# Kernel optimization log

Measured on AMD Instinct MI355X. Metric: run time of the kernel, lower is better.

The kernel has to match this reference:

```python
import jax, jax.numpy as jnp
import numpy as np

SHORT_LEN = 10
NEG_INF = -1.0e9


def _attn_pool(values, user, w, w_bias, extra_b, mask, softmax_axis):
    # values: [B,L,D], user: [B,D]; linear+bias+relu, dot with user, masked softmax, weighted sum
    h = jax.nn.relu(jnp.einsum('bld,ed->ble', values, w) + w_bias + extra_b)
    s = jnp.einsum('bld,bd->bl', h, user)
    s = jnp.where(mask, NEG_INF, s)
    a = jax.nn.softmax(s, axis=softmax_axis)
    return jnp.einsum('bld,bl->bd', values, a)


def setup_inputs() -> dict:
    key = jax.random.key(0)
    ks = jax.random.split(key, 10)
    B, L, D, NI, NU = 2048, 50, 64, 100000, 100000
    return {
        'seq': jax.random.randint(ks[0], (B, L), 0, NI),
        'user_id': jax.random.randint(ks[1], (B,), 0, NU),
        'item_emb': jax.random.normal(ks[2], (NI, D), jnp.float32) * 0.01,
        'user_emb': jax.random.normal(ks[3], (NU, D), jnp.float32) * 0.01,
        'long_w': jax.random.normal(ks[4], (D, D), jnp.float32) * 0.1,
        'long_w_bias': jax.random.normal(ks[5], (D,), jnp.float32) * 0.1,
        'long_b': jax.random.normal(ks[6], (D,), jnp.float32) * 0.1,
        'long_short_w': jax.random.normal(ks[7], (D, D), jnp.float32) * 0.1,
        'long_short_w_bias': jax.random.normal(ks[8], (D,), jnp.float32) * 0.1,
        'long_short_b': jax.random.normal(ks[9], (D,), jnp.float32) * 0.1,
    }


def reference(seq, user_id, item_emb, user_emb, long_w, long_w_bias, long_b,
              long_short_w, long_short_w_bias, long_short_b):
    e = item_emb[seq]                     # [B,L,D]
    u = user_emb[user_id]                 # [B,D]
    mask = seq == 0                       # padding mask
    # long-term attention pooling (softmax over dim=1)
    long_term = _attn_pool(e, u, long_w, long_w_bias, long_b, mask, 1)[:, None, :]  # [B,1,D]
    # concat long-term summary with last SHORT_LEN items
    short = e[:, -SHORT_LEN:, :]
    mask_ls = jnp.concatenate([jnp.zeros((seq.shape[0], 1), bool), mask[:, -SHORT_LEN:]], axis=1)
    ls = jnp.concatenate([long_term, short], axis=1)  # [B,1+K,D]
    pooled = _attn_pool(ls, u, long_short_w, long_short_w_bias, long_short_b, mask_ls, -1)  # [B,D]
    scores = pooled @ item_emb.T          # [B, n_items]
    return scores
```

## Files before the change

### kernel.cpp

```cpp
#include <hip/hip_runtime.h>
#include <hip/hip_bf16.h>


#define L_SEQ 50
#define D_EMB 64
#define SHORT_LEN 10
#define LS_LEN 11
#define NEG_INF_F (-1000000000.0f)
#define TILE_STRIP 16

typedef __bf16 bf16x8 __attribute__((ext_vector_type(8)));
typedef float f32x4 __attribute__((ext_vector_type(4)));

__device__ __forceinline__ float wave_sum(float v) {
#pragma unroll
  for (int off = 32; off > 0; off >>= 1) v += __shfl_xor(v, off, 64);
  return v;
}
__device__ __forceinline__ float wave_max(float v) {
#pragma unroll
  for (int off = 32; off > 0; off >>= 1) v = fmaxf(v, __shfl_xor(v, off, 64));
  return v;
}

__global__ __launch_bounds__(64) void pool_kernel(
    const int* __restrict__ seq, const int* __restrict__ user_id,
    const float* __restrict__ item_emb, const float* __restrict__ user_emb,
    const float* __restrict__ w1, const float* __restrict__ w1b, const float* __restrict__ b1,
    const float* __restrict__ w2, const float* __restrict__ w2b, const float* __restrict__ b2,
    float* __restrict__ pooled_f32, __bf16* __restrict__ pooled_bf) {
  const int b = blockIdx.x;
  const int lane = threadIdx.x;

  __shared__ float e_lds[L_SEQ][D_EMB];
  __shared__ float ls_lds[LS_LEN][D_EMB];
  __shared__ float a_lds[D_EMB];
  __shared__ int seq_lds[L_SEQ];

  if (lane < L_SEQ) seq_lds[lane] = seq[b * L_SEQ + lane];
  const float u = user_emb[(long)user_id[b] * D_EMB + lane];
  __syncthreads();

  for (int l = 0; l < L_SEQ; ++l) {
    e_lds[l][lane] = item_emb[(long)seq_lds[l] * D_EMB + lane];
  }

  float4 w1r[16];
#pragma unroll
  for (int k = 0; k < 16; ++k) w1r[k] = *(const float4*)&w1[lane * D_EMB + 4 * k];
  const float bias1 = w1b[lane] + b1[lane];
  __syncthreads();

  float s_val = 0.0f;
  for (int l = 0; l < L_SEQ; ++l) {
    float acc = bias1;
#pragma unroll
    for (int k = 0; k < 16; ++k) {
      float4 ev = *(const float4*)&e_lds[l][4 * k];
      acc = fmaf(ev.x, w1r[k].x, acc);
      acc = fmaf(ev.y, w1r[k].y, acc);
      acc = fmaf(ev.z, w1r[k].z, acc);
      acc = fmaf(ev.w, w1r[k].w, acc);
    }
    acc = fmaxf(acc, 0.0f);
    float t = wave_sum(acc * u);
    if (lane == l) s_val = (seq_lds[l] == 0) ? NEG_INF_F : t;
  }
  {
    float x = (lane < L_SEQ) ? s_val : -INFINITY;
    float m = wave_max(x);
    float p = (lane < L_SEQ) ? __expf(x - m) : 0.0f;
    float ps = wave_sum(p);
    a_lds[lane] = p / ps;
  }
  __syncthreads();

  float lt = 0.0f;
  for (int l = 0; l < L_SEQ; ++l) lt = fmaf(a_lds[l], e_lds[l][lane], lt);
  __syncthreads();

  ls_lds[0][lane] = lt;
#pragma unroll
  for (int j = 1; j < LS_LEN; ++j)
    ls_lds[j][lane] = e_lds[L_SEQ - SHORT_LEN + (j - 1)][lane];

  float4 w2r[16];
#pragma unroll
  for (int k = 0; k < 16; ++k) w2r[k] = *(const float4*)&w2[lane * D_EMB + 4 * k];
  const float bias2 = w2b[lane] + b2[lane];
  __syncthreads();

  float s2_val = 0.0f;
  for (int j = 0; j < LS_LEN; ++j) {
    float acc = bias2;
#pragma unroll
    for (int k = 0; k < 16; ++k) {
      float4 lv = *(const float4*)&ls_lds[j][4 * k];
      acc = fmaf(lv.x, w2r[k].x, acc);
      acc = fmaf(lv.y, w2r[k].y, acc);
      acc = fmaf(lv.z, w2r[k].z, acc);
      acc = fmaf(lv.w, w2r[k].w, acc);
    }
    acc = fmaxf(acc, 0.0f);
    float t = wave_sum(acc * u);
    bool msk = (j == 0) ? false : (seq_lds[L_SEQ - SHORT_LEN + (j - 1)] == 0);
    if (lane == j) s2_val = msk ? NEG_INF_F : t;
  }
  {
    float x = (lane < LS_LEN) ? s2_val : -INFINITY;
    float m = wave_max(x);
    float p = (lane < LS_LEN) ? __expf(x - m) : 0.0f;
    float ps = wave_sum(p);
    __syncthreads();
    a_lds[lane] = p / ps;
  }
  __syncthreads();

  float po = 0.0f;
#pragma unroll
  for (int j = 0; j < LS_LEN; ++j) po = fmaf(a_lds[j], ls_lds[j][lane], po);
  if (pooled_f32) pooled_f32[(long)b * D_EMB + lane] = po;
  if (pooled_bf) pooled_bf[(long)b * D_EMB + lane] = (__bf16)po;
}

__global__ __launch_bounds__(256) void cvt_bf16_kernel(
    const float* __restrict__ in, __bf16* __restrict__ out, int n8) {
  int i = blockIdx.x * blockDim.x + threadIdx.x;
  if (i >= n8) return;
  float4 a = ((const float4*)in)[2 * i];
  float4 b = ((const float4*)in)[2 * i + 1];
  bf16x8 v;
  v[0] = (__bf16)a.x; v[1] = (__bf16)a.y; v[2] = (__bf16)a.z; v[3] = (__bf16)a.w;
  v[4] = (__bf16)b.x; v[5] = (__bf16)b.y; v[6] = (__bf16)b.z; v[7] = (__bf16)b.w;
  ((bf16x8*)out)[i] = v;
}

__global__ __launch_bounds__(256) void scores_mfma_kernel(
    const __bf16* __restrict__ pooled_bf,
    const __bf16* __restrict__ item_bf,
    float* __restrict__ out, int NI, int n_tiles) {
  const int tid = threadIdx.x;
  const int w = tid >> 6;
  const int l = tid & 63;
  const int lr = l & 15;
  const int lg = l >> 4;
  const int b0 = blockIdx.y * 256 + w * 64;

  bf16x8 pfrag[4][2];
#pragma unroll
  for (int g = 0; g < 4; ++g) {
    const __bf16* prow = pooled_bf + (size_t)(b0 + 16 * g + lr) * D_EMB + 8 * lg;
    pfrag[g][0] = *(const bf16x8*)(prow);
    pfrag[g][1] = *(const bf16x8*)(prow + 32);
  }

  const int t_begin = blockIdx.x * TILE_STRIP;
  const int t_end = min(t_begin + TILE_STRIP, n_tiles);

#pragma unroll 2
  for (int t = t_begin; t < t_end; ++t) {
    const __bf16* brow = item_bf + (size_t)(t * 16 + lr) * D_EMB + 8 * lg;
    bf16x8 a0 = *(const bf16x8*)(brow);
    bf16x8 a1 = *(const bf16x8*)(brow + 32);

#pragma unroll
    for (int g = 0; g < 4; ++g) {
      f32x4 acc = {0.f, 0.f, 0.f, 0.f};
      acc = __builtin_amdgcn_mfma_f32_16x16x32_bf16(a0, pfrag[g][0], acc, 0, 0, 0);
      acc = __builtin_amdgcn_mfma_f32_16x16x32_bf16(a1, pfrag[g][1], acc, 0, 0, 0);
      float* op = out + (size_t)(b0 + 16 * g + lr) * NI + t * 16 + 4 * lg;
      __builtin_nontemporal_store(acc, (f32x4*)op);
    }
  }
}

__global__ __launch_bounds__(256) void scores_kernel(
    const float* __restrict__ pooled, const float* __restrict__ item_emb,
    float* __restrict__ out, int NI) {
  constexpr int STR = 68;
  __shared__ __align__(16) float poolT[64 * STR];
  __shared__ __align__(16) float itemT[64 * STR];

  const int tid = threadIdx.x;
  const int lane = tid & 63;
  const int b0 = blockIdx.x * 64;
  const int i0 = blockIdx.y * 64;

  for (int r = tid >> 6; r < 64; r += 4) {
    poolT[lane * STR + r] = pooled[(long)(b0 + r) * D_EMB + lane];
    int i = i0 + r;
    itemT[lane * STR + r] = (i < NI) ? item_emb[(long)i * D_EMB + lane] : 0.0f;
  }
  __syncthreads();

  const int tx = tid & 15;
  const int ty = tid >> 4;
  float acc[4][4] = {};

#pragma unroll 8
  for (int d = 0; d < 64; ++d) {
    float4 pv = *(const float4*)&poolT[d * STR + ty * 4];
    float4 iv = *(const float4*)&itemT[d * STR + tx * 4];
    float pva[4] = {pv.x, pv.y, pv.z, pv.w};
    float iva[4] = {iv.x, iv.y, iv.z, iv.w};
#pragma unroll
    for (int m = 0; m < 4; ++m)
#pragma unroll
      for (int n = 0; n < 4; ++n) acc[m][n] = fmaf(pva[m], iva[n], acc[m][n]);
  }

  const int ibase = i0 + tx * 4;
  const long orow = (long)(b0 + ty * 4);
  if (i0 + 63 < NI) {
#pragma unroll
    for (int m = 0; m < 4; ++m) {
      float4 v = make_float4(acc[m][0], acc[m][1], acc[m][2], acc[m][3]);
      *(float4*)&out[(orow + m) * (long)NI + ibase] = v;
    }
  } else {
#pragma unroll
    for (int m = 0; m < 4; ++m)
#pragma unroll
      for (int n = 0; n < 4; ++n)
        if (ibase + n < NI) out[(orow + m) * (long)NI + ibase + n] = acc[m][n];
  }
}

extern "C" void kernel_launch(void* const* d_in, const int* in_sizes, int n_in,
                              void* d_out, int out_size, void* d_ws, size_t ws_size,
                              hipStream_t stream) {
  const int* seq = (const int*)d_in[0];
  const int* user_id = (const int*)d_in[1];
  const float* item_emb = (const float*)d_in[2];
  const float* user_emb = (const float*)d_in[3];
  const float* w1 = (const float*)d_in[4];
  const float* w1b = (const float*)d_in[5];
  const float* b1 = (const float*)d_in[6];
  const float* w2 = (const float*)d_in[7];
  const float* w2b = (const float*)d_in[8];
  const float* b2 = (const float*)d_in[9];
  float* out = (float*)d_out;

  const int B = in_sizes[1];
  const int NI = in_sizes[2] / D_EMB;

  const size_t item_bf_bytes = (size_t)NI * D_EMB * 2;
  const size_t pooled_bf_bytes = (size_t)B * D_EMB * 2;
  const bool mfma_ok = (ws_size >= item_bf_bytes + pooled_bf_bytes) &&
                       (NI % 16 == 0) && (B % 256 == 0) && (D_EMB == 64);

  if (mfma_ok) {
    __bf16* item_bf = (__bf16*)d_ws;
    __bf16* pooled_bf = (__bf16*)((char*)d_ws + item_bf_bytes);

    const int n8 = NI * D_EMB / 8;
    cvt_bf16_kernel<<<(n8 + 255) / 256, 256, 0, stream>>>(item_emb, item_bf, n8);

    pool_kernel<<<B, 64, 0, stream>>>(seq, user_id, item_emb, user_emb,
                                      w1, w1b, b1, w2, w2b, b2,
                                      (float*)nullptr, pooled_bf);

    const int n_tiles = NI / 16;
    dim3 grid((n_tiles + TILE_STRIP - 1) / TILE_STRIP, B / 256);
    scores_mfma_kernel<<<grid, 256, 0, stream>>>(pooled_bf, item_bf, out, NI, n_tiles);
  } else {
    float* pooled = (float*)d_ws;
    pool_kernel<<<B, 64, 0, stream>>>(seq, user_id, item_emb, user_emb,
                                      w1, w1b, b1, w2, w2b, b2,
                                      pooled, (__bf16*)nullptr);
    dim3 grid(B / 64, (NI + 63) / 64);
    scores_kernel<<<grid, 256, 0, stream>>>(pooled, item_emb, out, NI);
  }
}
```

Before: 310.6 us.

## Restructure score GEMM blocks to sweep item quarters per 16-row user group

The score kernel now assigns each block one 16-row group of pooled users and a quarter of all item tiles, with the four waves interleaving over item tiles, instead of 256 users by a 16-tile item strip. Each block's output writes then fill long contiguous row segments, which should make the dominant output write stream more DRAM-friendly. In exchange each item tile is loaded once per 16 users rather than once per 64, so item traffic through L2 rises, and each wave holds a single pooled fragment.

```diff
diff --git a/kernel.cpp b/kernel.cpp
--- a/kernel.cpp
+++ b/kernel.cpp
@@ -7,7 +7,7 @@
 #define SHORT_LEN 10
 #define LS_LEN 11
 #define NEG_INF_F (-1000000000.0f)
-#define TILE_STRIP 16
+#define N_QUARTERS 4
 
 typedef __bf16 bf16x8 __attribute__((ext_vector_type(8)));
 typedef float f32x4 __attribute__((ext_vector_type(4)));
@@ -138,39 +138,34 @@
 __global__ __launch_bounds__(256) void scores_mfma_kernel(
     const __bf16* __restrict__ pooled_bf,
     const __bf16* __restrict__ item_bf,
-    float* __restrict__ out, int NI, int n_tiles) {
+    float* __restrict__ out, int NI, int n_tiles, int n_rowgrp, int qtiles) {
+  const int bid = blockIdx.x;
+  const int q = bid / n_rowgrp;
+  const int rg = bid % n_rowgrp;
   const int tid = threadIdx.x;
   const int w = tid >> 6;
   const int l = tid & 63;
   const int lr = l & 15;
   const int lg = l >> 4;
-  const int b0 = blockIdx.y * 256 + w * 64;
-
-  bf16x8 pfrag[4][2];
-#pragma unroll
-  for (int g = 0; g < 4; ++g) {
-    const __bf16* prow = pooled_bf + (size_t)(b0 + 16 * g + lr) * D_EMB + 8 * lg;
-    pfrag[g][0] = *(const bf16x8*)(prow);
-    pfrag[g][1] = *(const bf16x8*)(prow + 32);
-  }
-
-  const int t_begin = blockIdx.x * TILE_STRIP;
-  const int t_end = min(t_begin + TILE_STRIP, n_tiles);
-
-#pragma unroll 2
-  for (int t = t_begin; t < t_end; ++t) {
+  const int b0 = rg * 16;
+
+  const __bf16* prow = pooled_bf + (size_t)(b0 + lr) * D_EMB + 8 * lg;
+  bf16x8 pf0 = *(const bf16x8*)(prow);
+  bf16x8 pf1 = *(const bf16x8*)(prow + 32);
+
+  const int t_begin = q * qtiles;
+  const int t_end = min(t_begin + qtiles, n_tiles);
+
+#pragma unroll 4
+  for (int t = t_begin + w; t < t_end; t += 4) {
     const __bf16* brow = item_bf + (size_t)(t * 16 + lr) * D_EMB + 8 * lg;
     bf16x8 a0 = *(const bf16x8*)(brow);
     bf16x8 a1 = *(const bf16x8*)(brow + 32);
-
-#pragma unroll
-    for (int g = 0; g < 4; ++g) {
-      f32x4 acc = {0.f, 0.f, 0.f, 0.f};
-      acc = __builtin_amdgcn_mfma_f32_16x16x32_bf16(a0, pfrag[g][0], acc, 0, 0, 0);
-      acc = __builtin_amdgcn_mfma_f32_16x16x32_bf16(a1, pfrag[g][1], acc, 0, 0, 0);
-      float* op = out + (size_t)(b0 + 16 * g + lr) * NI + t * 16 + 4 * lg;
-      __builtin_nontemporal_store(acc, (f32x4*)op);
-    }
+    f32x4 acc = {0.f, 0.f, 0.f, 0.f};
+    acc = __builtin_amdgcn_mfma_f32_16x16x32_bf16(a0, pf0, acc, 0, 0, 0);
+    acc = __builtin_amdgcn_mfma_f32_16x16x32_bf16(a1, pf1, acc, 0, 0, 0);
+    float* op = out + (size_t)(b0 + lr) * NI + t * 16 + 4 * lg;
+    __builtin_nontemporal_store(acc, (f32x4*)op);
   }
 }
 
@@ -247,7 +242,7 @@
   const size_t item_bf_bytes = (size_t)NI * D_EMB * 2;
   const size_t pooled_bf_bytes = (size_t)B * D_EMB * 2;
   const bool mfma_ok = (ws_size >= item_bf_bytes + pooled_bf_bytes) &&
-                       (NI % 16 == 0) && (B % 256 == 0) && (D_EMB == 64);
+                       (NI % 16 == 0) && (B % 16 == 0) && (D_EMB == 64);
 
   if (mfma_ok) {
     __bf16* item_bf = (__bf16*)d_ws;
@@ -261,8 +256,10 @@
                                       (float*)nullptr, pooled_bf);
 
     const int n_tiles = NI / 16;
-    dim3 grid((n_tiles + TILE_STRIP - 1) / TILE_STRIP, B / 256);
-    scores_mfma_kernel<<<grid, 256, 0, stream>>>(pooled_bf, item_bf, out, NI, n_tiles);
+    const int n_rowgrp = B / 16;
+    const int qtiles = (n_tiles + N_QUARTERS - 1) / N_QUARTERS;
+    scores_mfma_kernel<<<N_QUARTERS * n_rowgrp, 256, 0, stream>>>(
+        pooled_bf, item_bf, out, NI, n_tiles, n_rowgrp, qtiles);
   } else {
     float* pooled = (float*)d_ws;
     pool_kernel<<<B, 64, 0, stream>>>(seq, user_id, item_emb, user_emb,
```

Result: faster. 272.8 us (-12.2%).
